# Kernel optimization log

Hardware: AMD Instinct MI355X
Metric: run time of the kernel (lower is better)

## Reference

```python
import jax, jax.numpy as jnp
import numpy as np

IOU_THRESH = 0.5
NEG_POS_RATIO = 3
VAR0, VAR1 = 0.1, 0.2  # BoxCoder variances


def box_iou(a, b):
    # a: [G,4] xyxy, b: [P,4] xyxy -> [G,P]
    lt = jnp.maximum(a[:, None, :2], b[None, :, :2])
    rb = jnp.minimum(a[:, None, 2:], b[None, :, 2:])
    wh = jnp.clip(rb - lt, 0.0)
    inter = wh[..., 0] * wh[..., 1]
    area_a = (a[:, 2] - a[:, 0]) * (a[:, 3] - a[:, 1])
    area_b = (b[:, 2] - b[:, 0]) * (b[:, 3] - b[:, 1])
    return inter / (area_a[:, None] + area_b[None, :] - inter)


def xywha_to_xyxy(p):
    c, wh = p[:, :2], p[:, 2:]
    return jnp.concatenate([c - wh * 0.5, c + wh * 0.5], axis=-1)


def assign_targets(gt_boxes, gt_labels, priors_xyxy):
    # gt_boxes [G,4], gt_labels [G], priors_xyxy [P,4]
    iou = box_iou(gt_boxes, priors_xyxy)            # [G,P]
    matched_vals = iou.max(axis=0)                  # [P]
    matches = iou.argmax(axis=0)                    # [P]
    best_prior = iou.argmax(axis=1)                 # [G] best prior per target
    G = gt_boxes.shape[0]
    matches = matches.at[best_prior].set(jnp.arange(G))
    matched_vals = matched_vals.at[best_prior].set(2.0)
    labels = jnp.where(matched_vals < IOU_THRESH, 0, gt_labels[matches])  # [P]
    boxes = gt_boxes[matches]                       # [P,4]
    return boxes, labels


def encode(boxes_xyxy, priors_xywha):
    # SSD center-form encoding with variances
    ctr = (boxes_xyxy[:, :2] + boxes_xyxy[:, 2:]) * 0.5
    wh = boxes_xyxy[:, 2:] - boxes_xyxy[:, :2]
    g_c = (ctr - priors_xywha[:, :2]) / (VAR0 * priors_xywha[:, 2:])
    g_wh = jnp.log(wh / priors_xywha[:, 2:]) / VAR1
    return jnp.concatenate([g_c, g_wh], axis=-1)


def hard_negative_mask(bg_loss, labels):
    # bg_loss [B,P]: -log_softmax(logits)[...,0]; keep all positives and
    # top-(ratio*num_pos) hardest negatives per image.
    pos = labels > 0
    num_neg = pos.sum(axis=1, keepdims=True) * NEG_POS_RATIO
    loss = jnp.where(pos, -jnp.inf, bg_loss)
    order = jnp.argsort(-loss, axis=1)
    rank = jnp.argsort(order, axis=1)
    return pos | (rank < num_neg)


def reference(priors, class_logits, box_regression, gt_boxes, gt_labels):
    priors_xyxy = xywha_to_xyxy(priors)
    boxes, labels = jax.vmap(assign_targets, in_axes=(0, 0, None))(
        gt_boxes, gt_labels, priors_xyxy)            # [B,P,4], [B,P]
    regression_targets = jax.vmap(encode, in_axes=(0, None))(boxes, priors)

    logp = jax.nn.log_softmax(class_logits, axis=-1)  # [B,P,C]
    bg_loss = jax.lax.stop_gradient(-logp[..., 0])
    mask = hard_negative_mask(bg_loss, labels)        # [B,P] bool

    # masked cross-entropy, reduction='sum'
    ce = -jnp.take_along_axis(logp, labels[..., None], axis=-1)[..., 0]
    loss_classifier = jnp.sum(jnp.where(mask, ce, 0.0))

    # masked smooth-L1 (beta=1), reduction='sum' over positives
    pos = labels > 0
    d = jnp.abs(box_regression - regression_targets)
    sl1 = jnp.where(d < 1.0, 0.5 * d * d, d - 0.5)
    loss_box_reg = jnp.sum(jnp.where(pos[..., None], sl1, 0.0))

    num_pos = jnp.sum(pos).astype(class_logits.dtype)
    return loss_box_reg / num_pos, loss_classifier / num_pos


def setup_inputs() -> dict:
    key = jax.random.key(0)
    ks = jax.random.split(key, 8)
    B, P, C, G = 64, 8732, 81, 16
    # priors: xywha in [0,1] with small positive wh
    p_c = jax.random.uniform(ks[0], (P, 2), jnp.float32, 0.05, 0.95)
    p_wh = jax.random.uniform(ks[1], (P, 2), jnp.float32, 0.02, 0.25)
    priors = jnp.concatenate([p_c, p_wh], axis=-1)
    class_logits = jax.random.normal(ks[2], (B, P, C), jnp.float32)
    box_regression = jax.random.normal(ks[3], (B, P, 4), jnp.float32)
    # gt boxes: valid xyxy in [0,1] with positive size
    g_c = jax.random.uniform(ks[4], (B, G, 2), jnp.float32, 0.2, 0.8)
    g_wh = jax.random.uniform(ks[5], (B, G, 2), jnp.float32, 0.05, 0.3)
    gt_boxes = jnp.concatenate([g_c - g_wh * 0.5, g_c + g_wh * 0.5], axis=-1)
    gt_labels = jax.random.randint(ks[6], (B, G), 1, C, jnp.int32)
    return {"priors": priors, "class_logits": class_logits,
            "box_regression": box_regression, "gt_boxes": gt_boxes,
            "gt_labels": gt_labels}
```

## Files before the change

### kernel.cpp

```cpp
#include <hip/hip_runtime.h>
#include <cfloat>

#define GT 16
#define NCLS 81
#define TPB 256
#define BPT 1024
#define MAXP 8732
#define TROWS 64

__device__ __forceinline__ float smoothl1(float d){
  float a = fabsf(d);
  return a < 1.0f ? 0.5f*a*a : a - 0.5f;
}

__global__ __launch_bounds__(BPT) void bestprior(
    const float* __restrict__ priors,
    const float* __restrict__ gt_boxes,
    int*   __restrict__ best,
    float* __restrict__ ce_pos, float* __restrict__ sl1_sum,
    int* __restrict__ num_pos, float* __restrict__ out, int P)
{
  const int b = blockIdx.x;
  const int tid = threadIdx.x, wave = tid >> 6, lane = tid & 63;
  __shared__ float gx0[GT], gy0[GT], gx1[GT], gy1[GT], ga[GT];
  __shared__ float redv[16*GT]; __shared__ int redi[16*GT];
  if (tid == 0){ ce_pos[b] = 0.0f; sl1_sum[b] = 0.0f; num_pos[b] = 0; }
  if (b == 0 && tid < 2) out[tid] = 0.0f;
  if (tid < GT){
    const float4 gb = ((const float4*)gt_boxes)[b*GT + tid];
    gx0[tid]=gb.x; gy0[tid]=gb.y; gx1[tid]=gb.z; gy1[tid]=gb.w;
    ga[tid] = (gb.z-gb.x)*(gb.w-gb.y);
  }
  __syncthreads();
  float bv[GT]; int bi[GT];
  #pragma unroll
  for (int g=0; g<GT; ++g){ bv[g] = -1.0f; bi[g] = 0x7fffffff; }
  for (int p = tid; p < P; p += BPT){
    const float4 pr = ((const float4*)priors)[p];
    const float px0 = pr.x - pr.z*0.5f, py0 = pr.y - pr.w*0.5f;
    const float px1 = pr.x + pr.z*0.5f, py1 = pr.y + pr.w*0.5f;
    const float pa = (px1-px0)*(py1-py0);
    #pragma unroll
    for (int g=0; g<GT; ++g){
      const float w = fmaxf(fminf(gx1[g],px1) - fmaxf(gx0[g],px0), 0.0f);
      const float h = fmaxf(fminf(gy1[g],py1) - fmaxf(gy0[g],py0), 0.0f);
      const float inter = w*h;
      const float iou = inter / (ga[g] + pa - inter);
      if (iou > bv[g]){ bv[g] = iou; bi[g] = p; }
    }
  }
  #pragma unroll
  for (int g=0; g<GT; ++g){
    float v = bv[g]; int i = bi[g];
    for (int off=32; off>0; off>>=1){
      const float ov = __shfl_down(v, off);
      const int   oi = __shfl_down(i, off);
      if (ov > v || (ov == v && oi < i)){ v = ov; i = oi; }
    }
    if (lane == 0){ redv[wave*GT+g] = v; redi[wave*GT+g] = i; }
  }
  __syncthreads();
  if (tid < GT){
    float v = redv[tid]; int i = redi[tid];
    for (int w=1; w<16; ++w){
      const float ov = redv[w*GT+tid]; const int oi = redi[w*GT+tid];
      if (ov > v || (ov == v && oi < i)){ v = ov; i = oi; }
    }
    best[b*GT + tid] = i;
  }
}

__global__ __launch_bounds__(TPB) void fused_lse(
    const float* __restrict__ priors,
    const float* __restrict__ gt_boxes,
    const int*   __restrict__ gt_labels,
    const float* __restrict__ box_reg,
    const int*   __restrict__ best,
    const float* __restrict__ logits,
    float* __restrict__ bg,
    float* __restrict__ ce_pos,
    float* __restrict__ sl1_sum,
    int*   __restrict__ num_pos,
    int P, int NT)
{
  __shared__ float sgx0[2][GT], sgy0[2][GT], sgx1[2][GT], sgy1[2][GT], sga[2][GT];
  __shared__ int   slab[2][GT], sbp[2][GT];
  const int tid = threadIdx.x;
  const int wave = tid >> 6, lane = tid & 63;
  const int rl = lane >> 2, q = lane & 3;
  const int G = gridDim.x;

  const int qn = NT / G, rn = NT % G;
  const int k = blockIdx.x;
  const int t0  = k < rn ? k*(qn+1) : rn*(qn+1) + (k-rn)*qn;
  const int cnt = k < rn ? qn+1 : qn;
  if (cnt <= 0) return;
  const int tend = t0 + cnt;
  const int b0 = (t0*TROWS)/P;
  const int b1 = (tend*TROWS - 1)/P;
  const int boundary = b1*P;

  if (tid < 2*GT){
    const int slot = tid >> 4, g = tid & 15;
    const int bb = slot ? b1 : b0;
    const float4 gb = ((const float4*)gt_boxes)[bb*GT + g];
    sgx0[slot][g]=gb.x; sgy0[slot][g]=gb.y; sgx1[slot][g]=gb.z; sgy1[slot][g]=gb.w;
    sga[slot][g] = (gb.z-gb.x)*(gb.w-gb.y);
    slab[slot][g] = gt_labels[bb*GT + g];
    sbp[slot][g]  = best[bb*GT + g];
  }
  __syncthreads();

  const int s = q*20;
  for (int t = t0; t < tend; ++t){
    const int row = t*TROWS + wave*16 + rl;
    const int slot = (row >= boundary);
    const int b = slot ? b1 : b0;
    const int p = row - b*P;
    const float* xr = logits + (long long)row*NCLS;

    float xv[21];
    #pragma unroll
    for (int j = 0; j < 21; ++j) xv[j] = xr[s + j];

    const float4 pr = ((const float4*)priors)[p];
    const float4 br = ((const float4*)box_reg)[row];

    const float px0 = pr.x - pr.z*0.5f, py0 = pr.y - pr.w*0.5f;
    const float px1 = pr.x + pr.z*0.5f, py1 = pr.y + pr.w*0.5f;
    const float pa  = (px1-px0)*(py1-py0);
    float mv = -1.0f; int mi = 0;
    const int gbase = q*4;
    #pragma unroll
    for (int j=0; j<4; ++j){
      const int g = gbase + j;
      const float w = fmaxf(fminf(sgx1[slot][g],px1) - fmaxf(sgx0[slot][g],px0), 0.0f);
      const float h = fmaxf(fminf(sgy1[slot][g],py1) - fmaxf(sgy0[slot][g],py0), 0.0f);
      const float inter = w*h;
      const float iou = inter / (sga[slot][g] + pa - inter);
      if (iou > mv){ mv = iou; mi = g; }
    }
    #pragma unroll
    for (int m=1; m<4; m<<=1){
      const float omv = __shfl_xor(mv, m);
      const int   omi = __shfl_xor(mi, m);
      if (omv > mv || (omv == mv && omi < mi)){ mv = omv; mi = omi; }
    }
    int ov = -1;
    #pragma unroll
    for (int j=0; j<4; ++j){
      const int g2 = gbase + j;
      if (sbp[slot][g2] == p) ov = g2;
    }
    #pragma unroll
    for (int m=1; m<4; m<<=1) ov = max(ov, __shfl_xor(ov, m));
    if (ov >= 0){ mv = 2.0f; mi = ov; }

    int lab = 0; float s1 = 0.0f;
    if (q == 0 && mv >= 0.5f){
      lab = slab[slot][mi];
      const float gbx0 = sgx0[slot][mi], gby0 = sgy0[slot][mi];
      const float gbx1 = sgx1[slot][mi], gby1 = sgy1[slot][mi];
      const float ctrx = (gbx0+gbx1)*0.5f, ctry = (gby0+gby1)*0.5f;
      const float wx = gbx1-gbx0, wy = gby1-gby0;
      const float tx = (ctrx - pr.x) / (0.1f*pr.z);
      const float ty = (ctry - pr.y) / (0.1f*pr.w);
      const float tw = __logf(wx/pr.z) / 0.2f;
      const float th = __logf(wy/pr.w) / 0.2f;
      s1 = smoothl1(br.x - tx) + smoothl1(br.y - ty)
         + smoothl1(br.z - tw) + smoothl1(br.w - th);
    }

    float sum = (q == 0) ? __expf(xv[0]) : 0.0f;
    #pragma unroll
    for (int j = 1; j < 21; ++j) sum += __expf(xv[j]);
    sum += __shfl_xor(sum, 1);
    sum += __shfl_xor(sum, 2);
    if (q == 0){
      const float lse = __logf(sum);
      float bgv;
      if (lab > 0){
        atomicAdd(&ce_pos[b], lse - xr[lab]);
        atomicAdd(&sl1_sum[b], s1);
        atomicAdd(&num_pos[b], 1);
        bgv = 0.0f;
      } else {
        bgv = fmaxf(lse - xv[0], 0.0f);
      }
      bg[row] = bgv;
    }
  }
}

__global__ __launch_bounds__(TPB) void topk_kernel(
    const float* __restrict__ bg,
    const int*   __restrict__ num_pos,
    const float* __restrict__ sl1_sum,
    const float* __restrict__ ce_pos,
    float* __restrict__ out,
    int P, int B)
{
  const int b = blockIdx.x;
  const int tid = threadIdx.x;
  const int wave = tid >> 6, lane = tid & 63;
  const int rep = tid & 15;
  __shared__ float sv[MAXP];
  __shared__ unsigned cntR[16][257];
  __shared__ unsigned s_wc[4];
  __shared__ float    s_wf[4];
  __shared__ unsigned s_prefix;
  __shared__ int s_krem, s_chosen, s_newk;

  {
    const float4* srcp = (const float4*)(bg + (long long)b * P);
    float4* dst = (float4*)sv;
    for (int j = tid; j < P/4; j += TPB) dst[j] = srcp[j];
  }
  if (tid == 0){
    const int k = 3*num_pos[b];
    s_krem = k < P ? k : P-1;
    s_prefix = 0u;
  }
  __syncthreads();

  for (int level=0; level<4; ++level){
    const int shift = 24 - 8*level;
    for (int i = tid; i < 16*257; i += TPB) ((unsigned*)cntR)[i] = 0u;
    __syncthreads();
    const unsigned pref = s_prefix;
    const int k = s_krem;
    for (int j = tid; j < P/4; j += TPB){
      const float4 f4 = ((const float4*)sv)[j];
      #pragma unroll
      for (int e=0; e<4; ++e){
        const unsigned key = __float_as_uint((&f4.x)[e]);
        const bool ok = (level == 0) || ((key >> (shift+8)) == pref);
        if (ok) atomicAdd(&cntR[rep][(key >> shift) & 255u], 1u);
      }
    }
    __syncthreads();
    const int rb = 255 - tid;
    unsigned c = 0;
    #pragma unroll
    for (int r=0; r<16; ++r) c += cntR[r][rb];
    unsigned cv = c;
    #pragma unroll
    for (int off=1; off<64; off<<=1){
      const unsigned oc = __shfl_up(cv, off);
      if (lane >= off) cv += oc;
    }
    if (lane == 63) s_wc[wave] = cv;
    __syncthreads();
    unsigned addc = 0;
    for (int w=0; w<4; ++w) if (w < wave) addc += s_wc[w];
    const unsigned S = cv - c + addc;
    if ((int)S <= k && k < (int)(S + c)){
      s_chosen = rb; s_newk = k - (int)S;
    }
    __syncthreads();
    if (tid == 0){
      s_krem = s_newk;
      s_prefix = (pref << 8) | (unsigned)s_chosen;
    }
    __syncthreads();
  }
  const unsigned T = s_prefix;
  float acc = 0.0f;
  for (int j = tid; j < P/4; j += TPB){
    const float4 f4 = ((const float4*)sv)[j];
    #pragma unroll
    for (int e=0; e<4; ++e){
      const float f = (&f4.x)[e];
      if (__float_as_uint(f) > T) acc += f;
    }
  }
  for (int off=32; off>0; off>>=1) acc += __shfl_down(acc, off);
  if (lane == 0) s_wf[wave] = acc;
  __syncthreads();
  if (tid < 64){
    float n = 0.0f;
    for (int i = tid; i < B; i += 64) n += (float)num_pos[i];
    for (int off=32; off>0; off>>=1) n += __shfl_down(n, off);
    if (tid == 0){
      const float N = n;
      const float cls = s_wf[0]+s_wf[1]+s_wf[2]+s_wf[3]
                      + (float)s_krem * __uint_as_float(T);
      atomicAdd(&out[0], sl1_sum[b] / N);
      atomicAdd(&out[1], (ce_pos[b] + cls) / N);
    }
  }
}

extern "C" void kernel_launch(void* const* d_in, const int* in_sizes, int n_in,
                              void* d_out, int out_size, void* d_ws, size_t ws_size,
                              hipStream_t stream) {
  const float* priors = (const float*)d_in[0];
  const float* logits = (const float*)d_in[1];
  const float* boxreg = (const float*)d_in[2];
  const float* gtb    = (const float*)d_in[3];
  const int*   gtl    = (const int*)d_in[4];
  const int P = in_sizes[0] / 4;
  const int B = in_sizes[4] / GT;
  const long long BP = (long long)B * P;

  char* ws = (char*)d_ws;
  float* bgv  = (float*)ws;
  int*   best = (int*)(ws + BP*4);
  float* sl1_s= (float*)(ws + BP*4 + 4096);
  int*   npos = (int*)  (ws + BP*4 + 4352);
  float* cep  = (float*)(ws + BP*4 + 4608);

  bestprior<<<B, BPT, 0, stream>>>(priors, gtb, best, cep, sl1_s, npos,
                                   (float*)d_out, P);
  const int NT = (int)(BP / TROWS);
  const int G = 2048;
  fused_lse<<<G, TPB, 0, stream>>>(priors, gtb, gtl, boxreg, best, logits,
                                   bgv, cep, sl1_s, npos, P, NT);
  topk_kernel<<<B, TPB, 0, stream>>>(bgv, npos, sl1_s, cep, (float*)d_out, P, B);
}
```

Before: 354.6 us.

## Map one logits row per lane with unaligned vector loads in fused_lse

Changes fused_lse from four lanes per row (each reading 20-21 strided scalars and combining via shuffles) to one lane per row. Each wave now owns whole 64-row tiles and the 4 waves stride over tiles. Each lane computes the IoU over all 16 GT boxes, the best-prior override and the full 81-class exp-sum itself, reading the row with memcpy-based float4 loads. This removes the cross-lane shuffles and the idle lanes in the epilogue, but neighbouring lanes now read addresses 324 bytes apart, so loads coalesce poorly, and per-thread work and register pressure go up.

```diff
diff --git a/kernel.cpp b/kernel.cpp
--- a/kernel.cpp
+++ b/kernel.cpp
@@ -11,6 +11,12 @@
 __device__ __forceinline__ float smoothl1(float d){
   float a = fabsf(d);
   return a < 1.0f ? 0.5f*a*a : a - 0.5f;
+}
+
+__device__ __forceinline__ float4 ld4u(const float* p){
+  float4 v;
+  __builtin_memcpy(&v, p, sizeof(float4));
+  return v;
 }
 
 __global__ __launch_bounds__(BPT) void bestprior(
@@ -87,7 +93,6 @@
   __shared__ int   slab[2][GT], sbp[2][GT];
   const int tid = threadIdx.x;
   const int wave = tid >> 6, lane = tid & 63;
-  const int rl = lane >> 2, q = lane & 3;
   const int G = gridDim.x;
 
   const int qn = NT / G, rn = NT % G;
@@ -111,18 +116,13 @@
   }
   __syncthreads();
 
-  const int s = q*20;
-  for (int t = t0; t < tend; ++t){
-    const int row = t*TROWS + wave*16 + rl;
+  for (int t = t0 + wave; t < tend; t += 4){
+    const int row = t*TROWS + lane;
     const int slot = (row >= boundary);
     const int b = slot ? b1 : b0;
     const int p = row - b*P;
     const float* xr = logits + (long long)row*NCLS;
 
-    float xv[21];
-    #pragma unroll
-    for (int j = 0; j < 21; ++j) xv[j] = xr[s + j];
-
     const float4 pr = ((const float4*)priors)[p];
     const float4 br = ((const float4*)box_reg)[row];
 
@@ -130,10 +130,8 @@
     const float px1 = pr.x + pr.z*0.5f, py1 = pr.y + pr.w*0.5f;
     const float pa  = (px1-px0)*(py1-py0);
     float mv = -1.0f; int mi = 0;
-    const int gbase = q*4;
-    #pragma unroll
-    for (int j=0; j<4; ++j){
-      const int g = gbase + j;
+    #pragma unroll
+    for (int g=0; g<GT; ++g){
       const float w = fmaxf(fminf(sgx1[slot][g],px1) - fmaxf(sgx0[slot][g],px0), 0.0f);
       const float h = fmaxf(fminf(sgy1[slot][g],py1) - fmaxf(sgy0[slot][g],py0), 0.0f);
       const float inter = w*h;
@@ -141,23 +139,11 @@
       if (iou > mv){ mv = iou; mi = g; }
     }
     #pragma unroll
-    for (int m=1; m<4; m<<=1){
-      const float omv = __shfl_xor(mv, m);
-      const int   omi = __shfl_xor(mi, m);
-      if (omv > mv || (omv == mv && omi < mi)){ mv = omv; mi = omi; }
-    }
-    int ov = -1;
-    #pragma unroll
-    for (int j=0; j<4; ++j){
-      const int g2 = gbase + j;
-      if (sbp[slot][g2] == p) ov = g2;
-    }
-    #pragma unroll
-    for (int m=1; m<4; m<<=1) ov = max(ov, __shfl_xor(ov, m));
-    if (ov >= 0){ mv = 2.0f; mi = ov; }
-
-    int lab = 0; float s1 = 0.0f;
-    if (q == 0 && mv >= 0.5f){
+    for (int g2=0; g2<GT; ++g2)
+      if (sbp[slot][g2] == p){ mv = 2.0f; mi = g2; }
+
+    int lab = 0; float sl1v = 0.0f;
+    if (mv >= 0.5f){
       lab = slab[slot][mi];
       const float gbx0 = sgx0[slot][mi], gby0 = sgy0[slot][mi];
       const float gbx1 = sgx1[slot][mi], gby1 = sgy1[slot][mi];
@@ -167,28 +153,61 @@
       const float ty = (ctry - pr.y) / (0.1f*pr.w);
       const float tw = __logf(wx/pr.z) / 0.2f;
       const float th = __logf(wy/pr.w) / 0.2f;
-      s1 = smoothl1(br.x - tx) + smoothl1(br.y - ty)
-         + smoothl1(br.z - tw) + smoothl1(br.w - th);
-    }
-
-    float sum = (q == 0) ? __expf(xv[0]) : 0.0f;
-    #pragma unroll
-    for (int j = 1; j < 21; ++j) sum += __expf(xv[j]);
-    sum += __shfl_xor(sum, 1);
-    sum += __shfl_xor(sum, 2);
-    if (q == 0){
-      const float lse = __logf(sum);
-      float bgv;
-      if (lab > 0){
-        atomicAdd(&ce_pos[b], lse - xr[lab]);
-        atomicAdd(&sl1_sum[b], s1);
-        atomicAdd(&num_pos[b], 1);
-        bgv = 0.0f;
-      } else {
-        bgv = fmaxf(lse - xv[0], 0.0f);
-      }
-      bg[row] = bgv;
-    }
+      sl1v = smoothl1(br.x - tx) + smoothl1(br.y - ty)
+           + smoothl1(br.z - tw) + smoothl1(br.w - th);
+    }
+
+    float4 a0 = ld4u(xr+ 0), a1 = ld4u(xr+ 4), a2 = ld4u(xr+ 8),
+           a3 = ld4u(xr+12), a4 = ld4u(xr+16);
+    const float x20 = xr[20];
+    const float x0v = a0.x;
+    float s0 = __expf(a0.x);
+    s0 += __expf(a0.y); s0 += __expf(a0.z); s0 += __expf(a0.w);
+    s0 += __expf(a1.x); s0 += __expf(a1.y); s0 += __expf(a1.z); s0 += __expf(a1.w);
+    s0 += __expf(a2.x); s0 += __expf(a2.y); s0 += __expf(a2.z); s0 += __expf(a2.w);
+    s0 += __expf(a3.x); s0 += __expf(a3.y); s0 += __expf(a3.z); s0 += __expf(a3.w);
+    s0 += __expf(a4.x); s0 += __expf(a4.y); s0 += __expf(a4.z); s0 += __expf(a4.w);
+    s0 += __expf(x20);
+
+    float4 c0 = ld4u(xr+21), c1 = ld4u(xr+25), c2 = ld4u(xr+29),
+           c3 = ld4u(xr+33), c4 = ld4u(xr+37);
+    float s1 = __expf(c0.x);
+    s1 += __expf(c0.y); s1 += __expf(c0.z); s1 += __expf(c0.w);
+    s1 += __expf(c1.x); s1 += __expf(c1.y); s1 += __expf(c1.z); s1 += __expf(c1.w);
+    s1 += __expf(c2.x); s1 += __expf(c2.y); s1 += __expf(c2.z); s1 += __expf(c2.w);
+    s1 += __expf(c3.x); s1 += __expf(c3.y); s1 += __expf(c3.z); s1 += __expf(c3.w);
+    s1 += __expf(c4.x); s1 += __expf(c4.y); s1 += __expf(c4.z); s1 += __expf(c4.w);
+
+    float4 d0 = ld4u(xr+41), d1 = ld4u(xr+45), d2 = ld4u(xr+49),
+           d3 = ld4u(xr+53), d4 = ld4u(xr+57);
+    float s2 = __expf(d0.x);
+    s2 += __expf(d0.y); s2 += __expf(d0.z); s2 += __expf(d0.w);
+    s2 += __expf(d1.x); s2 += __expf(d1.y); s2 += __expf(d1.z); s2 += __expf(d1.w);
+    s2 += __expf(d2.x); s2 += __expf(d2.y); s2 += __expf(d2.z); s2 += __expf(d2.w);
+    s2 += __expf(d3.x); s2 += __expf(d3.y); s2 += __expf(d3.z); s2 += __expf(d3.w);
+    s2 += __expf(d4.x); s2 += __expf(d4.y); s2 += __expf(d4.z); s2 += __expf(d4.w);
+
+    float4 e0 = ld4u(xr+61), e1 = ld4u(xr+65), e2 = ld4u(xr+69),
+           e3 = ld4u(xr+73), e4 = ld4u(xr+77);
+    float s3 = __expf(e0.x);
+    s3 += __expf(e0.y); s3 += __expf(e0.z); s3 += __expf(e0.w);
+    s3 += __expf(e1.x); s3 += __expf(e1.y); s3 += __expf(e1.z); s3 += __expf(e1.w);
+    s3 += __expf(e2.x); s3 += __expf(e2.y); s3 += __expf(e2.z); s3 += __expf(e2.w);
+    s3 += __expf(e3.x); s3 += __expf(e3.y); s3 += __expf(e3.z); s3 += __expf(e3.w);
+    s3 += __expf(e4.x); s3 += __expf(e4.y); s3 += __expf(e4.z); s3 += __expf(e4.w);
+
+    const float sum = (s0 + s1) + (s2 + s3);
+    const float lse = __logf(sum);
+    float bgv;
+    if (lab > 0){
+      atomicAdd(&ce_pos[b], lse - xr[lab]);
+      atomicAdd(&sl1_sum[b], sl1v);
+      atomicAdd(&num_pos[b], 1);
+      bgv = 0.0f;
+    } else {
+      bgv = fmaxf(lse - x0v, 0.0f);
+    }
+    bg[row] = bgv;
   }
 }
 
```

Result: slower. 377.3 us (+6.4%).

## Process four rows per wave with coalesced float4 logit loads and wave-wide LSE

Applied to the files above, without the earlier changes.

Restructures the fused log-sum-exp kernel so each wave handles a group of four contiguous rows (324 floats) with float4 coalesced loads instead of scalar per-lane loads of 21 elements. Exponential sums are split across the four row segments and reduced with full-wave shuffles. IoU matching now uses 16 lanes per row, one gt box each, with gt data held in registers. This targets memory-load efficiency on the dominant logits read, at the cost of more shuffle reductions. It also assumes P is divisible by 4 so a group never straddles two images.

```diff
diff --git a/kernel.cpp b/kernel.cpp
--- a/kernel.cpp
+++ b/kernel.cpp
@@ -6,7 +6,6 @@
 #define TPB 256
 #define BPT 1024
 #define MAXP 8732
-#define TROWS 64
 
 __device__ __forceinline__ float smoothl1(float d){
   float a = fabsf(d);
@@ -81,24 +80,24 @@
     float* __restrict__ ce_pos,
     float* __restrict__ sl1_sum,
     int*   __restrict__ num_pos,
-    int P, int NT)
+    int P, int NG)
 {
   __shared__ float sgx0[2][GT], sgy0[2][GT], sgx1[2][GT], sgy1[2][GT], sga[2][GT];
   __shared__ int   slab[2][GT], sbp[2][GT];
   const int tid = threadIdx.x;
   const int wave = tid >> 6, lane = tid & 63;
-  const int rl = lane >> 2, q = lane & 3;
   const int G = gridDim.x;
 
-  const int qn = NT / G, rn = NT % G;
-  const int k = blockIdx.x;
-  const int t0  = k < rn ? k*(qn+1) : rn*(qn+1) + (k-rn)*qn;
-  const int cnt = k < rn ? qn+1 : qn;
+  const int qn = NG / G, rn = NG % G;
+  const int kb = blockIdx.x;
+  const int t0  = kb < rn ? kb*(qn+1) : rn*(qn+1) + (kb-rn)*qn;
+  const int cnt = kb < rn ? qn+1 : qn;
   if (cnt <= 0) return;
   const int tend = t0 + cnt;
-  const int b0 = (t0*TROWS)/P;
-  const int b1 = (tend*TROWS - 1)/P;
-  const int boundary = b1*P;
+  const int GP = P >> 2;
+  const int b0 = t0 / GP;
+  const int b1 = (tend - 1) / GP;
+  const int boundary_g = b1 * GP;
 
   if (tid < 2*GT){
     const int slot = tid >> 4, g = tid & 15;
@@ -111,83 +110,119 @@
   }
   __syncthreads();
 
-  const int s = q*20;
-  for (int t = t0; t < tend; ++t){
-    const int row = t*TROWS + wave*16 + rl;
-    const int slot = (row >= boundary);
+  const int L  = lane >> 4;
+  const int sq = lane & 15;
+  const float Agx0 = sgx0[0][sq], Agy0 = sgy0[0][sq],
+              Agx1 = sgx1[0][sq], Agy1 = sgy1[0][sq], Aga = sga[0][sq];
+  const float Bgx0 = sgx0[1][sq], Bgy0 = sgy0[1][sq],
+              Bgx1 = sgx1[1][sq], Bgy1 = sgy1[1][sq], Bga = sga[1][sq];
+  const int Abp = sbp[0][sq], Bbp = sbp[1][sq];
+
+  const int lf0 = lane * 4;
+  const int r_lo = (lf0 >= 81) + (lf0 >= 162) + (lf0 >= 243);
+  const int bound = 81 * (r_lo + 1);
+  const float4* lg4 = (const float4*)logits;
+
+  for (int t = t0 + wave; t < tend; t += 4){
+    const int slot = (t >= boundary_g);
     const int b = slot ? b1 : b0;
-    const int p = row - b*P;
-    const float* xr = logits + (long long)row*NCLS;
-
-    float xv[21];
-    #pragma unroll
-    for (int j = 0; j < 21; ++j) xv[j] = xr[s + j];
-
+    const int g0row = t * 4;
+    const int pbase = g0row - b * P;
+    const long long fbase = 81LL * t;
+
+    float4 v = lg4[fbase + lane];
+    float4 v2;
+    if (lane < 17) v2 = lg4[fbase + 64 + lane];
+
+    const int p = pbase + L;
     const float4 pr = ((const float4*)priors)[p];
-    const float4 br = ((const float4*)box_reg)[row];
+    const float4 br = ((const float4*)box_reg)[g0row + L];
+
+    float lo = 0.0f, hi = 0.0f;
+    { const float e = __expf(v.x); if (lf0+0 >= bound) hi += e; else lo += e; }
+    { const float e = __expf(v.y); if (lf0+1 >= bound) hi += e; else lo += e; }
+    { const float e = __expf(v.z); if (lf0+2 >= bound) hi += e; else lo += e; }
+    { const float e = __expf(v.w); if (lf0+3 >= bound) hi += e; else lo += e; }
+    float s2 = 0.0f;
+    if (lane < 17)
+      s2 = __expf(v2.x) + __expf(v2.y) + __expf(v2.z) + __expf(v2.w);
+
+    float a0 = (r_lo == 0) ? lo : 0.0f;
+    float a1 = (r_lo == 0) ? hi : ((r_lo == 1) ? lo : 0.0f);
+    float a2 = (r_lo == 1) ? hi : ((r_lo == 2) ? lo : 0.0f);
+    float a3 = ((r_lo == 2) ? hi : ((r_lo == 3) ? lo : 0.0f)) + s2;
+
+    #pragma unroll
+    for (int m = 1; m < 64; m <<= 1){
+      a0 += __shfl_xor(a0, m);
+      a1 += __shfl_xor(a1, m);
+      a2 += __shfl_xor(a2, m);
+      a3 += __shfl_xor(a3, m);
+    }
+
+    float cand = v.x;
+    if (lane == 20) cand = v.y;
+    else if (lane == 40) cand = v.z;
+    else if (lane == 60) cand = v.w;
+    const float x00 = __shfl(cand, 0);
+    const float x01 = __shfl(cand, 20);
+    const float x02 = __shfl(cand, 40);
+    const float x03 = __shfl(cand, 60);
+
+    const float l0 = __logf(a0), l1 = __logf(a1),
+                l2 = __logf(a2), l3 = __logf(a3);
+
+    const float gx0v = slot ? Bgx0 : Agx0, gy0v = slot ? Bgy0 : Agy0;
+    const float gx1v = slot ? Bgx1 : Agx1, gy1v = slot ? Bgy1 : Agy1;
+    const float gav  = slot ? Bga  : Aga;
+    const int   bpv  = slot ? Bbp  : Abp;
 
     const float px0 = pr.x - pr.z*0.5f, py0 = pr.y - pr.w*0.5f;
     const float px1 = pr.x + pr.z*0.5f, py1 = pr.y + pr.w*0.5f;
     const float pa  = (px1-px0)*(py1-py0);
-    float mv = -1.0f; int mi = 0;
-    const int gbase = q*4;
-    #pragma unroll
-    for (int j=0; j<4; ++j){
-      const int g = gbase + j;
-      const float w = fmaxf(fminf(sgx1[slot][g],px1) - fmaxf(sgx0[slot][g],px0), 0.0f);
-      const float h = fmaxf(fminf(sgy1[slot][g],py1) - fmaxf(sgy0[slot][g],py0), 0.0f);
-      const float inter = w*h;
-      const float iou = inter / (sga[slot][g] + pa - inter);
-      if (iou > mv){ mv = iou; mi = g; }
-    }
-    #pragma unroll
-    for (int m=1; m<4; m<<=1){
+    const float w = fmaxf(fminf(gx1v,px1) - fmaxf(gx0v,px0), 0.0f);
+    const float h = fmaxf(fminf(gy1v,py1) - fmaxf(gy0v,py0), 0.0f);
+    const float inter = w*h;
+    float mv = inter / (gav + pa - inter);
+    int mi = sq;
+    #pragma unroll
+    for (int m = 1; m < 16; m <<= 1){
       const float omv = __shfl_xor(mv, m);
       const int   omi = __shfl_xor(mi, m);
       if (omv > mv || (omv == mv && omi < mi)){ mv = omv; mi = omi; }
     }
-    int ov = -1;
-    #pragma unroll
-    for (int j=0; j<4; ++j){
-      const int g2 = gbase + j;
-      if (sbp[slot][g2] == p) ov = g2;
-    }
-    #pragma unroll
-    for (int m=1; m<4; m<<=1) ov = max(ov, __shfl_xor(ov, m));
-    if (ov >= 0){ mv = 2.0f; mi = ov; }
-
-    int lab = 0; float s1 = 0.0f;
-    if (q == 0 && mv >= 0.5f){
-      lab = slab[slot][mi];
-      const float gbx0 = sgx0[slot][mi], gby0 = sgy0[slot][mi];
-      const float gbx1 = sgx1[slot][mi], gby1 = sgy1[slot][mi];
-      const float ctrx = (gbx0+gbx1)*0.5f, ctry = (gby0+gby1)*0.5f;
-      const float wx = gbx1-gbx0, wy = gby1-gby0;
-      const float tx = (ctrx - pr.x) / (0.1f*pr.z);
-      const float ty = (ctry - pr.y) / (0.1f*pr.w);
-      const float tw = __logf(wx/pr.z) / 0.2f;
-      const float th = __logf(wy/pr.w) / 0.2f;
-      s1 = smoothl1(br.x - tx) + smoothl1(br.y - ty)
-         + smoothl1(br.z - tw) + smoothl1(br.w - th);
-    }
-
-    float sum = (q == 0) ? __expf(xv[0]) : 0.0f;
-    #pragma unroll
-    for (int j = 1; j < 21; ++j) sum += __expf(xv[j]);
-    sum += __shfl_xor(sum, 1);
-    sum += __shfl_xor(sum, 2);
-    if (q == 0){
-      const float lse = __logf(sum);
-      float bgv;
+    int ovr = (bpv == p) ? sq : -1;
+    #pragma unroll
+    for (int m = 1; m < 16; m <<= 1) ovr = max(ovr, __shfl_xor(ovr, m));
+    if (ovr >= 0){ mv = 2.0f; mi = ovr; }
+
+    if (sq == 0){
+      const float lseL = (L==0) ? l0 : (L==1) ? l1 : (L==2) ? l2 : l3;
+      const float x0L  = (L==0) ? x00 : (L==1) ? x01 : (L==2) ? x02 : x03;
+      int lab = 0; float sl1v = 0.0f;
+      if (mv >= 0.5f){
+        lab = slab[slot][mi];
+        const float gbx0 = sgx0[slot][mi], gby0 = sgy0[slot][mi];
+        const float gbx1 = sgx1[slot][mi], gby1 = sgy1[slot][mi];
+        const float ctrx = (gbx0+gbx1)*0.5f, ctry = (gby0+gby1)*0.5f;
+        const float wx = gbx1-gbx0, wy = gby1-gby0;
+        const float tx = (ctrx - pr.x) / (0.1f*pr.z);
+        const float ty = (ctry - pr.y) / (0.1f*pr.w);
+        const float tw = __logf(wx/pr.z) / 0.2f;
+        const float th = __logf(wy/pr.w) / 0.2f;
+        sl1v = smoothl1(br.x - tx) + smoothl1(br.y - ty)
+             + smoothl1(br.z - tw) + smoothl1(br.w - th);
+      }
+      float outv;
       if (lab > 0){
-        atomicAdd(&ce_pos[b], lse - xr[lab]);
-        atomicAdd(&sl1_sum[b], s1);
+        atomicAdd(&ce_pos[b], lseL - logits[(long long)(g0row+L)*NCLS + lab]);
+        atomicAdd(&sl1_sum[b], sl1v);
         atomicAdd(&num_pos[b], 1);
-        bgv = 0.0f;
+        outv = 0.0f;
       } else {
-        bgv = fmaxf(lse - xv[0], 0.0f);
+        outv = fmaxf(lseL - x0L, 0.0f);
       }
-      bg[row] = bgv;
+      bg[g0row + L] = outv;
     }
   }
 }
@@ -312,9 +347,9 @@
 
   bestprior<<<B, BPT, 0, stream>>>(priors, gtb, best, cep, sl1_s, npos,
                                    (float*)d_out, P);
-  const int NT = (int)(BP / TROWS);
+  const int NG = (int)(BP / 4);
   const int G = 2048;
   fused_lse<<<G, TPB, 0, stream>>>(priors, gtb, gtl, boxreg, best, logits,
-                                   bgv, cep, sl1_s, npos, P, NT);
+                                   bgv, cep, sl1_s, npos, P, NG);
   topk_kernel<<<B, TPB, 0, stream>>>(bgv, npos, sl1_s, cep, (float*)d_out, P, B);
 }
```

Result: slower. 364.6 us (+2.8%).
